# Optimization experiments

Measured on AMD Instinct MI355X. Metric: run time of the kernel, lower is better.

The kernel has to match this reference:

```python
import jax, jax.numpy as jnp
import numpy as np

VOCAB = 30000
N_NODES = 10000
N_EDGES = 160000
D = 1024


def setup_inputs() -> dict:
    key = jax.random.key(0)
    ks = jax.random.split(key, 10)
    s = 1.0 / np.sqrt(D)
    return {
        "node": jax.random.randint(ks[0], (N_NODES,), 0, VOCAB),
        "src": jax.random.randint(ks[1], (N_EDGES,), 0, N_NODES),
        "dst": jax.random.randint(ks[2], (N_EDGES,), 0, N_NODES),
        "emb": jax.random.normal(ks[3], (VOCAB, D), jnp.float32),
        "W1_self": jax.random.uniform(ks[4], (D, D), jnp.float32, -s, s),
        "W1_neigh": jax.random.uniform(ks[5], (D, D), jnp.float32, -s, s),
        "b1": jax.random.uniform(ks[6], (D,), jnp.float32, -s, s),
        "W2_self": jax.random.uniform(ks[7], (D, D), jnp.float32, -s, s),
        "W2_neigh": jax.random.uniform(ks[8], (D, D), jnp.float32, -s, s),
        "b2": jax.random.uniform(ks[9], (D,), jnp.float32, -s, s),
    }


def _sage_conv(h, src, dst, W_self, W_neigh, b):
    # DGL SAGEConv 'mean': mean over in-neighbors (src -> dst), 0 for isolated dst
    n = h.shape[0]
    deg = jax.ops.segment_sum(jnp.ones((src.shape[0],), h.dtype), dst, num_segments=n)
    agg = jax.ops.segment_sum(h[src], dst, num_segments=n)  # [n, D]
    h_neigh = agg / jnp.maximum(deg, 1.0)[:, None]
    # rst = fc_self(h) + fc_neigh(h_neigh); fc_self has no bias in DGL
    return h @ W_self + h_neigh @ W_neigh + b


def reference(node, src, dst, emb, W1_self, W1_neigh, b1, W2_self, W2_neigh, b2):
    x = emb[node]  # [N_NODES, D] embedding lookup
    h = jax.nn.relu(_sage_conv(x, src, dst, W1_self, W1_neigh, b1))
    return _sage_conv(h, src, dst, W2_self, W2_neigh, b2)
```

## Files before the change

kernel.cpp:

```cpp
#include <hip/hip_runtime.h>
#include <hip/hip_bf16.h>

#define N_NODES 10000
#define N_EDGES 160000
#define DD 1024
#define KCAT 2048
#define MPAD 10240
#define MTILES 79
#define NTILES 8
#define NBLK (MTILES * NTILES)

typedef __attribute__((ext_vector_type(8))) __bf16 bf16x8;
typedef __attribute__((ext_vector_type(4))) __bf16 bf16x4;
typedef __attribute__((ext_vector_type(4))) float f32x4;

__device__ inline void gload_lds16(const void* g, void* l) {
  __builtin_amdgcn_global_load_lds((const __attribute__((address_space(1))) void*)g,
                                   (__attribute__((address_space(3))) void*)l, 16, 0, 0);
}

__global__ __launch_bounds__(256) void k_hist(const int* __restrict__ dst,
                                              int* __restrict__ deg) {
  int e = blockIdx.x * 256 + threadIdx.x;
  if (e < N_EDGES) atomicAdd(&deg[dst[e]], 1);
}

__global__ __launch_bounds__(1024) void k_scan(const int* __restrict__ deg,
                                               int* __restrict__ off) {
  int t = threadIdx.x;
  int base_i = t * 10;
  int loc[10];
  int sum = 0;
#pragma unroll
  for (int j = 0; j < 10; ++j) {
    int idx = base_i + j;
    int v = (idx < N_NODES) ? deg[idx] : 0;
    loc[j] = sum;
    sum += v;
  }
  int lane = t & 63, w = t >> 6;
  int inc = sum;
#pragma unroll
  for (int d = 1; d < 64; d <<= 1) {
    int y = __shfl_up(inc, d);
    if (lane >= d) inc += y;
  }
  __shared__ int wtot[16];
  __shared__ int wpre[16];
  if (lane == 63) wtot[w] = inc;
  __syncthreads();
  if (t == 0) {
    int c = 0;
    for (int k = 0; k < 16; ++k) { wpre[k] = c; c += wtot[k]; }
    off[N_NODES] = c;
  }
  __syncthreads();
  int tbase = wpre[w] + (inc - sum);
#pragma unroll
  for (int j = 0; j < 10; ++j) {
    int idx = base_i + j;
    if (idx < N_NODES) off[idx] = tbase + loc[j];
  }
}

__global__ __launch_bounds__(256) void k_fill(const int* __restrict__ src,
                                              const int* __restrict__ dst,
                                              const int* __restrict__ off,
                                              int* __restrict__ cursor,
                                              int* __restrict__ eidx) {
  int e = blockIdx.x * 256 + threadIdx.x;
  if (e < N_EDGES) {
    int d = dst[e];
    int pos = atomicAdd(&cursor[d], 1);
    eidx[off[d] + pos] = src[e];
  }
}

__global__ __launch_bounds__(256) void k_embed(const int* __restrict__ node,
                                               const float* __restrict__ emb,
                                               __bf16* __restrict__ xcat) {
  int i = blockIdx.x;
  int t = threadIdx.x;
  float4 v = ((const float4*)(emb + (size_t)node[i] * DD))[t];
  bf16x4 o;
  o[0] = (__bf16)v.x; o[1] = (__bf16)v.y; o[2] = (__bf16)v.z; o[3] = (__bf16)v.w;
  *(bf16x4*)(xcat + (size_t)i * KCAT + t * 4) = o;
}

__global__ __launch_bounds__(256) void k_wconv(const float* __restrict__ Ws,
                                               const float* __restrict__ Wn,
                                               __bf16* __restrict__ Wt) {
  __shared__ float tile[32][33];
  int k0 = blockIdx.x * 32;
  int c0 = blockIdx.y * 32;
  for (int i = threadIdx.y; i < 32; i += 8) {
    int k = k0 + i, c = c0 + threadIdx.x;
    float v = (k < DD) ? Ws[(size_t)k * DD + c] : Wn[(size_t)(k - DD) * DD + c];
    tile[i][threadIdx.x] = v;
  }
  __syncthreads();
  for (int i = threadIdx.y; i < 32; i += 8) {
    int c = c0 + i, k = k0 + threadIdx.x;
    Wt[(size_t)c * KCAT + k] = (__bf16)tile[threadIdx.x][i];
  }
}

__global__ __launch_bounds__(256) void k_agg(__bf16* __restrict__ buf,
                                             const int* __restrict__ off,
                                             const int* __restrict__ eidx) {
  int wid = blockIdx.x * 4 + (threadIdx.x >> 6);
  if (wid >= N_NODES) return;
  int lane = threadIdx.x & 63;
  int s = off[wid], e = off[wid + 1];
  size_t col = (size_t)lane * 16;
  float acc0[16], acc1[16];
#pragma unroll
  for (int j = 0; j < 16; ++j) { acc0[j] = 0.f; acc1[j] = 0.f; }
  int i = s;
  for (; i + 2 <= e; i += 2) {
    const __bf16* r0 = buf + (size_t)eidx[i] * KCAT + col;
    const __bf16* r1 = buf + (size_t)eidx[i + 1] * KCAT + col;
    bf16x8 u0 = *(const bf16x8*)r0;
    bf16x8 u1 = *(const bf16x8*)(r0 + 8);
    bf16x8 v0 = *(const bf16x8*)r1;
    bf16x8 v1 = *(const bf16x8*)(r1 + 8);
#pragma unroll
    for (int j = 0; j < 8; ++j) {
      acc0[j]     += (float)u0[j];
      acc0[8 + j] += (float)u1[j];
      acc1[j]     += (float)v0[j];
      acc1[8 + j] += (float)v1[j];
    }
  }
  if (i < e) {
    const __bf16* r0 = buf + (size_t)eidx[i] * KCAT + col;
    bf16x8 u0 = *(const bf16x8*)r0;
    bf16x8 u1 = *(const bf16x8*)(r0 + 8);
#pragma unroll
    for (int j = 0; j < 8; ++j) { acc0[j] += (float)u0[j]; acc0[8 + j] += (float)u1[j]; }
  }
  float inv = 1.0f / fmaxf((float)(e - s), 1.0f);
  bf16x8 o0, o1;
#pragma unroll
  for (int j = 0; j < 8; ++j) {
    o0[j] = (__bf16)((acc0[j] + acc1[j]) * inv);
    o1[j] = (__bf16)((acc0[8 + j] + acc1[8 + j]) * inv);
  }
  __bf16* dstp = buf + (size_t)wid * KCAT + DD + col;
  *(bf16x8*)dstp = o0;
  *(bf16x8*)(dstp + 8) = o1;
}

template <int MODE>
__global__ __launch_bounds__(256, 2) void k_gemm(const __bf16* __restrict__ A,
                                                 const __bf16* __restrict__ Bt,
                                                 const float* __restrict__ bias,
                                                 float* __restrict__ Cf,
                                                 __bf16* __restrict__ Cb,
                                                 int Mreal) {
  __shared__ char smem[65536];
  const int tid  = threadIdx.x;
  const int lane = tid & 63;
  const int w    = tid >> 6;
  const int wr   = w >> 1, wc = w & 1;
  const int b  = blockIdx.x;
  const int l  = (b & 7) * MTILES + (b >> 3);
  const int m0 = (l >> 3) * 128;
  const int n0 = (l & 7) * 128;

  f32x4 acc[4][4];
#pragma unroll
  for (int m = 0; m < 4; ++m)
#pragma unroll
    for (int n = 0; n < 4; ++n) acc[m][n] = f32x4{0.f, 0.f, 0.f, 0.f};

  int sr[4], sk[4];
#pragma unroll
  for (int i = 0; i < 4; ++i) {
    int G = (4 * w + i) * 64 + lane;
    int E = G ^ ((G >> 3) & 7);
    sr[i] = E >> 3;
    sk[i] = (E & 7) * 8;
  }

  auto stage = [&](int buf, int kt) {
    char* As = smem + buf * 32768;
    char* Bs = As + 16384;
#pragma unroll
    for (int i = 0; i < 4; ++i) {
      gload_lds16(A + (size_t)(m0 + sr[i]) * KCAT + (kt + sk[i]), As + (4 * w + i) * 1024);
      gload_lds16(Bt + (size_t)(n0 + sr[i]) * KCAT + (kt + sk[i]), Bs + (4 * w + i) * 1024);
    }
  };

  auto compute = [&](int buf) {
    char* As = smem + buf * 32768;
    char* Bs = As + 16384;
#pragma unroll
    for (int kk = 0; kk < 64; kk += 32) {
      const int koff = kk + ((lane >> 4) * 8);
      bf16x8 af[4], bfr[4];
#pragma unroll
      for (int m = 0; m < 4; ++m) {
        int r = wr * 64 + m * 16 + (lane & 15);
        int byte = ((r * 64 + koff) * 2) ^ ((r & 7) << 4);
        af[m] = *(const bf16x8*)(As + byte);
      }
#pragma unroll
      for (int n = 0; n < 4; ++n) {
        int c = wc * 64 + n * 16 + (lane & 15);
        int byte = ((c * 64 + koff) * 2) ^ ((c & 7) << 4);
        bfr[n] = *(const bf16x8*)(Bs + byte);
      }
#pragma unroll
      for (int m = 0; m < 4; ++m)
#pragma unroll
        for (int n = 0; n < 4; ++n)
          acc[m][n] = __builtin_amdgcn_mfma_f32_16x16x32_bf16(af[m], bfr[n], acc[m][n], 0, 0, 0);
    }
  };

  stage(0, 0);
  __syncthreads();
  int cur = 0;
  for (int kt = 0; kt < KCAT; kt += 64) {
    if (kt + 64 < KCAT) stage(cur ^ 1, kt + 64);
    compute(cur);
    __syncthreads();
    cur ^= 1;
  }

  const int rb = m0 + wr * 64;
  const int cb = n0 + wc * 64;
#pragma unroll
  for (int m = 0; m < 4; ++m) {
#pragma unroll
    for (int n = 0; n < 4; ++n) {
      int c = cb + n * 16 + (lane & 15);
      float bv = bias[c];
#pragma unroll
      for (int j = 0; j < 4; ++j) {
        int r = rb + m * 16 + (lane >> 4) * 4 + j;
        if (r < Mreal) {
          float v = acc[m][n][j] + bv;
          if constexpr (MODE == 1) {
            v = fmaxf(v, 0.f);
            Cb[(size_t)r * KCAT + c] = (__bf16)v;
          } else {
            Cf[(size_t)r * DD + c] = v;
          }
        }
      }
    }
  }
}

extern "C" void kernel_launch(void* const* d_in, const int* in_sizes, int n_in,
                              void* d_out, int out_size, void* d_ws, size_t ws_size,
                              hipStream_t stream) {
  const int*   node = (const int*)d_in[0];
  const int*   srcv = (const int*)d_in[1];
  const int*   dstv = (const int*)d_in[2];
  const float* emb  = (const float*)d_in[3];
  const float* W1s  = (const float*)d_in[4];
  const float* W1n  = (const float*)d_in[5];
  const float* b1   = (const float*)d_in[6];
  const float* W2s  = (const float*)d_in[7];
  const float* W2n  = (const float*)d_in[8];
  const float* b2   = (const float*)d_in[9];
  float* out = (float*)d_out;

  char* ws = (char*)d_ws;
  __bf16* xcat = (__bf16*)ws; ws += (size_t)MPAD * KCAT * 2;
  __bf16* hcat = (__bf16*)ws; ws += (size_t)MPAD * KCAT * 2;
  __bf16* Wt1  = (__bf16*)ws; ws += (size_t)DD * KCAT * 2;
  __bf16* Wt2  = (__bf16*)ws; ws += (size_t)DD * KCAT * 2;
  int* deg    = (int*)ws; ws += 40960;
  int* cursor = (int*)ws; ws += 40960;
  int* off    = (int*)ws; ws += 40960;
  int* eidx   = (int*)ws; ws += (size_t)N_EDGES * 4;

  hipMemsetAsync(deg, 0, N_NODES * sizeof(int), stream);
  hipMemsetAsync(cursor, 0, N_NODES * sizeof(int), stream);

  k_hist<<<(N_EDGES + 255) / 256, 256, 0, stream>>>(dstv, deg);
  k_scan<<<1, 1024, 0, stream>>>(deg, off);
  k_fill<<<(N_EDGES + 255) / 256, 256, 0, stream>>>(srcv, dstv, off, cursor, eidx);

  k_embed<<<N_NODES, 256, 0, stream>>>(node, emb, xcat);
  k_wconv<<<dim3(64, 32), dim3(32, 8), 0, stream>>>(W1s, W1n, Wt1);
  k_wconv<<<dim3(64, 32), dim3(32, 8), 0, stream>>>(W2s, W2n, Wt2);

  k_agg<<<2500, 256, 0, stream>>>(xcat, off, eidx);
  k_gemm<1><<<NBLK, 256, 0, stream>>>(xcat, Wt1, b1, nullptr, hcat, N_NODES);

  k_agg<<<2500, 256, 0, stream>>>(hcat, off, eidx);
  k_gemm<0><<<NBLK, 256, 0, stream>>>(hcat, Wt2, b2, out, nullptr, N_NODES);
}
```

Measured before the change: 457.5 us.

## Split neighbor aggregation by column slices with grid-stride node loop

Reworks the mean-aggregation kernel so each block handles one 128-column slice and waves stride over nodes, each lane accumulating two columns. This aims to improve cache locality of the gathered rows per slice and lower register pressure compared to per-lane 16-column accumulation. It trades wide 32-byte loads for narrow 4-byte loads and repeats the index reads across slices. The two workspace memsets are also merged into one.

```diff
diff --git a/kernel.cpp b/kernel.cpp
--- a/kernel.cpp
+++ b/kernel.cpp
@@ -9,6 +9,9 @@
 #define MTILES 79
 #define NTILES 8
 #define NBLK (MTILES * NTILES)
+
+#define AGG_BLOCKS 1000
+#define AGG_WPS 500
 
 typedef __attribute__((ext_vector_type(8))) __bf16 bf16x8;
 typedef __attribute__((ext_vector_type(4))) __bf16 bf16x4;
@@ -108,47 +111,33 @@
 __global__ __launch_bounds__(256) void k_agg(__bf16* __restrict__ buf,
                                              const int* __restrict__ off,
                                              const int* __restrict__ eidx) {
-  int wid = blockIdx.x * 4 + (threadIdx.x >> 6);
-  if (wid >= N_NODES) return;
-  int lane = threadIdx.x & 63;
-  int s = off[wid], e = off[wid + 1];
-  size_t col = (size_t)lane * 16;
-  float acc0[16], acc1[16];
-#pragma unroll
-  for (int j = 0; j < 16; ++j) { acc0[j] = 0.f; acc1[j] = 0.f; }
-  int i = s;
-  for (; i + 2 <= e; i += 2) {
-    const __bf16* r0 = buf + (size_t)eidx[i] * KCAT + col;
-    const __bf16* r1 = buf + (size_t)eidx[i + 1] * KCAT + col;
-    bf16x8 u0 = *(const bf16x8*)r0;
-    bf16x8 u1 = *(const bf16x8*)(r0 + 8);
-    bf16x8 v0 = *(const bf16x8*)r1;
-    bf16x8 v1 = *(const bf16x8*)(r1 + 8);
-#pragma unroll
-    for (int j = 0; j < 8; ++j) {
-      acc0[j]     += (float)u0[j];
-      acc0[8 + j] += (float)u1[j];
-      acc1[j]     += (float)v0[j];
-      acc1[8 + j] += (float)v1[j];
-    }
-  }
-  if (i < e) {
-    const __bf16* r0 = buf + (size_t)eidx[i] * KCAT + col;
-    bf16x8 u0 = *(const bf16x8*)r0;
-    bf16x8 u1 = *(const bf16x8*)(r0 + 8);
-#pragma unroll
-    for (int j = 0; j < 8; ++j) { acc0[j] += (float)u0[j]; acc0[8 + j] += (float)u1[j]; }
-  }
-  float inv = 1.0f / fmaxf((float)(e - s), 1.0f);
-  bf16x8 o0, o1;
-#pragma unroll
-  for (int j = 0; j < 8; ++j) {
-    o0[j] = (__bf16)((acc0[j] + acc1[j]) * inv);
-    o1[j] = (__bf16)((acc0[8 + j] + acc1[8 + j]) * inv);
-  }
-  __bf16* dstp = buf + (size_t)wid * KCAT + DD + col;
-  *(bf16x8*)dstp = o0;
-  *(bf16x8*)(dstp + 8) = o1;
+  const int s    = blockIdx.x & 7;
+  const int q    = blockIdx.x >> 3;
+  const int lane = threadIdx.x & 63;
+  const int w    = threadIdx.x >> 6;
+  const int wid  = q * 4 + w;
+  const size_t colb = (size_t)s * 128 + lane * 2;
+
+  for (int n = wid; n < N_NODES; n += AGG_WPS) {
+    int s0 = off[n], e0 = off[n + 1];
+    float a0 = 0.f, a1 = 0.f, b0 = 0.f, b1 = 0.f;
+    int i = s0;
+    for (; i + 2 <= e0; i += 2) {
+      const __bf16* r0 = buf + (size_t)eidx[i] * KCAT + colb;
+      const __bf16* r1 = buf + (size_t)eidx[i + 1] * KCAT + colb;
+      a0 += (float)r0[0]; a1 += (float)r0[1];
+      b0 += (float)r1[0]; b1 += (float)r1[1];
+    }
+    if (i < e0) {
+      const __bf16* r0 = buf + (size_t)eidx[i] * KCAT + colb;
+      a0 += (float)r0[0]; a1 += (float)r0[1];
+    }
+    float inv = 1.0f / fmaxf((float)(e0 - s0), 1.0f);
+    __bf16 o0 = (__bf16)((a0 + b0) * inv);
+    __bf16 o1 = (__bf16)((a1 + b1) * inv);
+    __bf16* dstp = buf + (size_t)n * KCAT + DD + colb;
+    dstp[0] = o0; dstp[1] = o1;
+  }
 }
 
 template <int MODE>
@@ -280,8 +269,7 @@
   int* off    = (int*)ws; ws += 40960;
   int* eidx   = (int*)ws; ws += (size_t)N_EDGES * 4;
 
-  hipMemsetAsync(deg, 0, N_NODES * sizeof(int), stream);
-  hipMemsetAsync(cursor, 0, N_NODES * sizeof(int), stream);
+  hipMemsetAsync(deg, 0, 2 * 40960, stream);
 
   k_hist<<<(N_EDGES + 255) / 256, 256, 0, stream>>>(dstv, deg);
   k_scan<<<1, 1024, 0, stream>>>(deg, off);
@@ -291,9 +279,9 @@
   k_wconv<<<dim3(64, 32), dim3(32, 8), 0, stream>>>(W1s, W1n, Wt1);
   k_wconv<<<dim3(64, 32), dim3(32, 8), 0, stream>>>(W2s, W2n, Wt2);
 
-  k_agg<<<2500, 256, 0, stream>>>(xcat, off, eidx);
+  k_agg<<<AGG_BLOCKS, 256, 0, stream>>>(xcat, off, eidx);
   k_gemm<1><<<NBLK, 256, 0, stream>>>(xcat, Wt1, b1, nullptr, hcat, N_NODES);
 
-  k_agg<<<2500, 256, 0, stream>>>(hcat, off, eidx);
+  k_agg<<<AGG_BLOCKS, 256, 0, stream>>>(hcat, off, eidx);
   k_gemm<0><<<NBLK, 256, 0, stream>>>(hcat, Wt2, b2, out, nullptr, N_NODES);
 }
```

Result: slower. 518.7 us (+13.4%).
